# Performance work log

Hardware: AMD Instinct MI355X
Metric: run time of the kernel (lower is better)

## Reference

```python
import jax, jax.numpy as jnp
import numpy as np

N_NODES = 50000
N_EDGES = 600000
F_IN = 128
HID = 128
LN_EPS = 1e-5


def setup_inputs() -> dict:
    key = jax.random.key(0)
    ks = jax.random.split(key, 8)
    x = jax.random.normal(ks[0], (N_NODES, F_IN), dtype=jnp.float32)
    edge_index = jax.random.randint(ks[1], (2, N_EDGES), 0, N_NODES, dtype=jnp.int64)
    s1 = 1.0 / np.sqrt(F_IN)
    s2 = 1.0 / np.sqrt(HID)
    return {
        "x": x,
        "edge_index": edge_index,
        "W1": jax.random.normal(ks[2], (F_IN, HID), dtype=jnp.float32) * s1,
        "b1": jnp.zeros((HID,), dtype=jnp.float32),
        "g1": jnp.ones((HID,), dtype=jnp.float32),
        "be1": jnp.zeros((HID,), dtype=jnp.float32),
        "W2": jax.random.normal(ks[3], (HID, HID), dtype=jnp.float32) * s2,
        "b2": jnp.zeros((HID,), dtype=jnp.float32),
        "g2": jnp.ones((HID,), dtype=jnp.float32),
        "be2": jnp.zeros((HID,), dtype=jnp.float32),
    }


def _layer_norm(h, g, b):
    mu = jnp.mean(h, axis=-1, keepdims=True)
    var = jnp.mean(jnp.square(h - mu), axis=-1, keepdims=True)
    return (h - mu) * jax.lax.rsqrt(var + LN_EPS) * g + b


def reference(x, edge_index, W1, b1, g1, be1, W2, b2, g2, be2):
    n = x.shape[0]
    src, dst = edge_index[0], edge_index[1]
    # GCN symmetric normalization with self-loops: deg = in-degree(A) + 1
    deg = jax.ops.segment_sum(jnp.ones_like(src, dtype=x.dtype), dst, num_segments=n) + 1.0
    dinv = jax.lax.rsqrt(deg)                       # D^{-1/2}, [N]
    enorm = (dinv[src] * dinv[dst])[:, None]        # per-edge norm, [E,1]
    self_norm = (dinv * dinv)[:, None]              # self-loop norm,  [N,1]

    def gcn(h, W, b):
        h = h @ W                                   # [N,HID]
        agg = jax.ops.segment_sum(h[src] * enorm, dst, num_segments=n)
        return agg + h * self_norm + b

    h = jax.nn.relu(_layer_norm(gcn(x, W1, b1), g1, be1))
    h = jax.nn.relu(_layer_norm(gcn(h, W2, b2), g2, be2))
    return h  # dropout is identity in eval; LSTM evolution only runs in training
```

## Files before the change

### kernel.cpp

```cpp
#include <hip/hip_runtime.h>

#define N_NODES 50000
#define N_EDGES 600000
#define HID 128
#define LN_EPS 1e-5f
#define NB_GEMM1 782
#define NB_HIST 2344

typedef __attribute__((ext_vector_type(8))) short short8;
typedef __attribute__((ext_vector_type(4))) float f32x4;

__device__ inline float b2f(unsigned short u) {
    union { unsigned int i; float f; } v;
    v.i = ((unsigned int)u) << 16;
    return v.f;
}
__device__ inline unsigned short f2b(float f) {
    union { float f; unsigned int u; } v; v.f = f;
    unsigned int r = (v.u + 0x7FFFu + ((v.u >> 16) & 1u)) >> 16;
    return (unsigned short)r;
}

__global__ __launch_bounds__(256) void k_fused1(const float* __restrict__ x,
                                                const float* __restrict__ W1,
                                                const float* __restrict__ W2,
                                                const int* __restrict__ ei,
                                                int* __restrict__ counts,
                                                unsigned short* __restrict__ WT2,
                                                unsigned short* __restrict__ hb) {
    const int tid = threadIdx.x;

    if (blockIdx.x >= NB_GEMM1) {
        const int bi = blockIdx.x - NB_GEMM1;
        const int e = bi * 256 + tid;
        if (e < N_EDGES) atomicAdd(&counts[ei[N_EDGES + e]], 1);
        if (bi < 64) {
            const int i = bi * 256 + tid;
            const int k = i >> 7, n = i & 127;
            WT2[n * 128 + k] = f2b(W2[i]);
        }
        return;
    }

    __shared__ unsigned short wt[16384];
    {
        const float4* W4 = (const float4*)W1;
#pragma unroll
        for (int it = 0; it < 16; ++it) {
            const int i4 = tid + 256 * it;
            const float4 v = W4[i4];
            const int k  = (i4 * 4) >> 7;
            const int n0 = (i4 * 4) & 127;
            wt[(n0 + 0) * 128 + (k ^ (((n0 + 0) & 7) << 3))] = f2b(v.x);
            wt[(n0 + 1) * 128 + (k ^ (((n0 + 1) & 7) << 3))] = f2b(v.y);
            wt[(n0 + 2) * 128 + (k ^ (((n0 + 2) & 7) << 3))] = f2b(v.z);
            wt[(n0 + 3) * 128 + (k ^ (((n0 + 3) & 7) << 3))] = f2b(v.w);
        }
    }
    __syncthreads();

    const int lane = tid & 63;
    const int ln   = lane & 15;
    const int quad = lane >> 4;
    const int m0   = blockIdx.x * 64 + (tid >> 6) * 16;

    f32x4 acc[8];
#pragma unroll
    for (int t = 0; t < 8; ++t) acc[t] = (f32x4){0.f, 0.f, 0.f, 0.f};

    int arow = m0 + ln;
    if (arow >= N_NODES) arow = N_NODES - 1;
    const float* aptr = x + (size_t)arow * HID + quad * 8;

#pragma unroll
    for (int ks = 0; ks < 4; ++ks) {
        const float4 v0 = *(const float4*)(aptr + ks * 32);
        const float4 v1 = *(const float4*)(aptr + ks * 32 + 4);
        short8 a;
        a[0] = (short)f2b(v0.x); a[1] = (short)f2b(v0.y);
        a[2] = (short)f2b(v0.z); a[3] = (short)f2b(v0.w);
        a[4] = (short)f2b(v1.x); a[5] = (short)f2b(v1.y);
        a[6] = (short)f2b(v1.z); a[7] = (short)f2b(v1.w);
#pragma unroll
        for (int t = 0; t < 8; ++t) {
            const int n = t * 16 + ln;
            const short8 b = *(const short8*)&wt[n * 128 + ((quad * 8 + ks * 32) ^ ((n & 7) << 3))];
            acc[t] = __builtin_amdgcn_mfma_f32_16x16x32_bf16(a, b, acc[t], 0, 0, 0);
        }
    }

#pragma unroll
    for (int t = 0; t < 8; ++t) {
#pragma unroll
        for (int r = 0; r < 4; ++r) {
            const int row = m0 + quad * 4 + r;
            if (row < N_NODES) hb[(size_t)row * HID + t * 16 + ln] = f2b(acc[t][r]);
        }
    }
}

__global__ __launch_bounds__(256) void k_slab(const int* __restrict__ counts,
                                              int* __restrict__ gtotal,
                                              int* __restrict__ slab,
                                              float* __restrict__ dinv) {
    const int idx  = blockIdx.x * 256 + threadIdx.x;
    const int lane = threadIdx.x & 63;
    const int c = (idx < N_NODES) ? counts[idx] : 0;

    int incl = c;
#pragma unroll
    for (int off = 1; off < 64; off <<= 1) {
        int n = __shfl_up(incl, off);
        if (lane >= off) incl += n;
    }
    const int wtot = __shfl(incl, 63);
    int base = 0;
    if (lane == 0) base = atomicAdd(gtotal, wtot);
    base = __shfl(base, 0);

    if (idx < N_NODES) {
        slab[idx] = base + incl - c;
        dinv[idx] = rsqrtf((float)c + 1.0f);
    }
}

__global__ __launch_bounds__(256) void k_place(const int* __restrict__ ei,
                                               int* __restrict__ slab,
                                               int* __restrict__ esrc) {
    int e = blockIdx.x * 256 + threadIdx.x;
    if (e < N_EDGES) {
        const int d = ei[N_EDGES + e];
        const int pos = atomicAdd(&slab[d], 1);
        esrc[pos] = ei[e];
    }
}

template <bool FUSE>
__global__ __launch_bounds__(256) void k_agg(const int* __restrict__ slab_end,
                                             const int* __restrict__ counts,
                                             const int* __restrict__ esrc,
                                             const unsigned short* __restrict__ h,
                                             const float* __restrict__ dinv,
                                             const float* __restrict__ bia,
                                             const float* __restrict__ g,
                                             const float* __restrict__ be,
                                             const unsigned short* __restrict__ WT2,
                                             unsigned short* __restrict__ hb2,
                                             float* __restrict__ outf) {
    __shared__ unsigned short tile[2048];
    const int tid  = threadIdx.x;
    const int wv   = tid >> 6;
    const int lane = tid & 63;
    const int grp  = lane >> 4;
    const int fl   = lane & 15;
    const int r    = wv * 4 + grp;
    const int row  = blockIdx.x * 16 + r;

    const int e1 = slab_end[row];
    const int e0 = e1 - counts[row];

    float acc[8];
#pragma unroll
    for (int j = 0; j < 8; ++j) acc[j] = 0.f;

    int e = e0;
    for (; e + 1 < e1; e += 2) {
        const int sA = esrc[e];
        const int sB = esrc[e + 1];
        const float wA = dinv[sA];
        const float wB = dinv[sB];
        const short8 vA = *(const short8*)(h + (size_t)sA * HID + 8 * fl);
        const short8 vB = *(const short8*)(h + (size_t)sB * HID + 8 * fl);
#pragma unroll
        for (int j = 0; j < 8; ++j) {
            acc[j] = fmaf(wA, b2f((unsigned short)vA[j]), acc[j]);
            acc[j] = fmaf(wB, b2f((unsigned short)vB[j]), acc[j]);
        }
    }
    if (e < e1) {
        const int sA = esrc[e];
        const float wA = dinv[sA];
        const short8 vA = *(const short8*)(h + (size_t)sA * HID + 8 * fl);
#pragma unroll
        for (int j = 0; j < 8; ++j)
            acc[j] = fmaf(wA, b2f((unsigned short)vA[j]), acc[j]);
    }

    const float dd = dinv[row];
    const float sn = dd * dd;
    const short8 hv = *(const short8*)(h + (size_t)row * HID + 8 * fl);
    const float4 b0 = *(const float4*)(bia + 8 * fl);
    const float4 b1 = *(const float4*)(bia + 8 * fl + 4);
    const float bb[8] = {b0.x, b0.y, b0.z, b0.w, b1.x, b1.y, b1.z, b1.w};

    float v[8], s = 0.f, ss = 0.f;
#pragma unroll
    for (int j = 0; j < 8; ++j) {
        v[j] = dd * acc[j] + b2f((unsigned short)hv[j]) * sn + bb[j];
        s += v[j];
        ss = fmaf(v[j], v[j], ss);
    }

#pragma unroll
    for (int off = 1; off <= 8; off <<= 1) {
        s  += __shfl_xor(s, off);
        ss += __shfl_xor(ss, off);
    }
    const float mu  = s * (1.0f / 128.0f);
    const float var = ss * (1.0f / 128.0f) - mu * mu;
    const float rs  = rsqrtf(var + LN_EPS);

    const float4 g0  = *(const float4*)(g + 8 * fl);
    const float4 g1  = *(const float4*)(g + 8 * fl + 4);
    const float4 e0v = *(const float4*)(be + 8 * fl);
    const float4 e1v = *(const float4*)(be + 8 * fl + 4);
    const float gg[8] = {g0.x, g0.y, g0.z, g0.w, g1.x, g1.y, g1.z, g1.w};
    const float ee[8] = {e0v.x, e0v.y, e0v.z, e0v.w, e1v.x, e1v.y, e1v.z, e1v.w};
    float o[8];
#pragma unroll
    for (int j = 0; j < 8; ++j)
        o[j] = fmaxf((v[j] - mu) * rs * gg[j] + ee[j], 0.0f);

    if constexpr (!FUSE) {
        float4 w0 = {o[0], o[1], o[2], o[3]};
        float4 w1 = {o[4], o[5], o[6], o[7]};
        *(float4*)(outf + (size_t)row * HID + 8 * fl) = w0;
        *(float4*)(outf + (size_t)row * HID + 8 * fl + 4) = w1;
    } else {
        short8 w;
#pragma unroll
        for (int j = 0; j < 8; ++j) w[j] = (short)f2b(o[j]);
        *(short8*)&tile[r * 128 + ((8 * fl) ^ ((r & 7) << 3))] = w;
        __syncthreads();

        f32x4 c0 = (f32x4){0.f, 0.f, 0.f, 0.f};
        f32x4 c1 = (f32x4){0.f, 0.f, 0.f, 0.f};
        const int n0 = (wv * 2) * 16 + fl;
#pragma unroll
        for (int ks = 0; ks < 4; ++ks) {
            const short8 a = *(const short8*)&tile[fl * 128 + ((grp * 8 + ks * 32) ^ ((fl & 7) << 3))];
            const short8 bf0 = *(const short8*)(WT2 + (size_t)n0 * HID + grp * 8 + ks * 32);
            c0 = __builtin_amdgcn_mfma_f32_16x16x32_bf16(a, bf0, c0, 0, 0, 0);
            const short8 bf1 = *(const short8*)(WT2 + (size_t)(n0 + 16) * HID + grp * 8 + ks * 32);
            c1 = __builtin_amdgcn_mfma_f32_16x16x32_bf16(a, bf1, c1, 0, 0, 0);
        }
#pragma unroll
        for (int rr = 0; rr < 4; ++rr) {
            const int orow = blockIdx.x * 16 + grp * 4 + rr;
            hb2[(size_t)orow * HID + n0]      = f2b(c0[rr]);
            hb2[(size_t)orow * HID + n0 + 16] = f2b(c1[rr]);
        }
    }
}

extern "C" void kernel_launch(void* const* d_in, const int* in_sizes, int n_in,
                              void* d_out, int out_size, void* d_ws, size_t ws_size,
                              hipStream_t stream) {
    (void)in_sizes; (void)n_in; (void)out_size; (void)ws_size;

    const float* x   = (const float*)d_in[0];
    const int*   ei  = (const int*)d_in[1];
    const float* W1  = (const float*)d_in[2];
    const float* b1  = (const float*)d_in[3];
    const float* g1  = (const float*)d_in[4];
    const float* be1 = (const float*)d_in[5];
    const float* W2  = (const float*)d_in[6];
    const float* b2  = (const float*)d_in[7];
    const float* g2  = (const float*)d_in[8];
    const float* be2 = (const float*)d_in[9];
    float* out = (float*)d_out;

    int* counts = (int*)d_ws;
    int* gtotal = counts + N_NODES;
    int* slab   = (int*)d_ws + 50016;
    float* dinv = (float*)((int*)d_ws + 100016);
    int* esrc   = (int*)d_ws + 150016;
    unsigned short* WT2 = (unsigned short*)((int*)d_ws + 750016);
    unsigned short* hb  = (unsigned short*)((int*)d_ws + 758208);
    unsigned short* hb2 = (unsigned short*)((int*)d_ws + 3958208);

    hipMemsetAsync(counts, 0, (N_NODES + 1) * sizeof(int), stream);
    k_fused1<<<NB_GEMM1 + NB_HIST, 256, 0, stream>>>(x, W1, W2, ei, counts, WT2, hb);
    k_slab<<<(N_NODES + 255) / 256, 256, 0, stream>>>(counts, gtotal, slab, dinv);
    k_place<<<NB_HIST, 256, 0, stream>>>(ei, slab, esrc);

    k_agg<true><<<N_NODES / 16, 256, 0, stream>>>(slab, counts, esrc, hb, dinv,
                                                  b1, g1, be1, WT2, hb2, nullptr);
    k_agg<false><<<N_NODES / 16, 256, 0, stream>>>(slab, counts, esrc, hb2, dinv,
                                                   b2, g2, be2, nullptr, nullptr, out);
}
```

Baseline: 223.7 us.

## Merge all stages into one persistent kernel with grid-wide barriers

Replaces the five separate kernel launches (GEMM+histogram, scan, placement, two aggregation layers) with a single persistent kernel of 512 blocks that loops over work and uses atomic-counter grid barriers between phases. This removes launch overhead and inter-kernel gaps. In exchange, the GEMM and aggregation work is spread over fewer blocks with grid-stride loops, and the software barriers rely on all 512 blocks being co-resident. Spin-waiting and reduced parallelism per phase could hurt throughput.

New measurement: 566.7 us. 2.53x slower.

```diff
diff --git a/kernel.cpp b/kernel.cpp
--- a/kernel.cpp
+++ b/kernel.cpp
@@ -4,8 +4,10 @@
 #define N_EDGES 600000
 #define HID 128
 #define LN_EPS 1e-5f
-#define NB_GEMM1 782
-#define NB_HIST 2344
+#define GRID 512
+#define NTHREADS (GRID * 256)
+#define NB_GEMM 782
+#define NTILES 3125
 
 typedef __attribute__((ext_vector_type(8))) short short8;
 typedef __attribute__((ext_vector_type(4))) float f32x4;
@@ -21,140 +23,38 @@
     return (unsigned short)r;
 }
 
-__global__ __launch_bounds__(256) void k_fused1(const float* __restrict__ x,
-                                                const float* __restrict__ W1,
-                                                const float* __restrict__ W2,
-                                                const int* __restrict__ ei,
-                                                int* __restrict__ counts,
-                                                unsigned short* __restrict__ WT2,
-                                                unsigned short* __restrict__ hb) {
-    const int tid = threadIdx.x;
-
-    if (blockIdx.x >= NB_GEMM1) {
-        const int bi = blockIdx.x - NB_GEMM1;
-        const int e = bi * 256 + tid;
-        if (e < N_EDGES) atomicAdd(&counts[ei[N_EDGES + e]], 1);
-        if (bi < 64) {
-            const int i = bi * 256 + tid;
-            const int k = i >> 7, n = i & 127;
-            WT2[n * 128 + k] = f2b(W2[i]);
-        }
-        return;
-    }
-
-    __shared__ unsigned short wt[16384];
-    {
-        const float4* W4 = (const float4*)W1;
-#pragma unroll
-        for (int it = 0; it < 16; ++it) {
-            const int i4 = tid + 256 * it;
-            const float4 v = W4[i4];
-            const int k  = (i4 * 4) >> 7;
-            const int n0 = (i4 * 4) & 127;
-            wt[(n0 + 0) * 128 + (k ^ (((n0 + 0) & 7) << 3))] = f2b(v.x);
-            wt[(n0 + 1) * 128 + (k ^ (((n0 + 1) & 7) << 3))] = f2b(v.y);
-            wt[(n0 + 2) * 128 + (k ^ (((n0 + 2) & 7) << 3))] = f2b(v.z);
-            wt[(n0 + 3) * 128 + (k ^ (((n0 + 3) & 7) << 3))] = f2b(v.w);
-        }
-    }
+__device__ inline void gsync(int* bar, int target) {
     __syncthreads();
-
-    const int lane = tid & 63;
-    const int ln   = lane & 15;
-    const int quad = lane >> 4;
-    const int m0   = blockIdx.x * 64 + (tid >> 6) * 16;
-
-    f32x4 acc[8];
-#pragma unroll
-    for (int t = 0; t < 8; ++t) acc[t] = (f32x4){0.f, 0.f, 0.f, 0.f};
-
-    int arow = m0 + ln;
-    if (arow >= N_NODES) arow = N_NODES - 1;
-    const float* aptr = x + (size_t)arow * HID + quad * 8;
-
-#pragma unroll
-    for (int ks = 0; ks < 4; ++ks) {
-        const float4 v0 = *(const float4*)(aptr + ks * 32);
-        const float4 v1 = *(const float4*)(aptr + ks * 32 + 4);
-        short8 a;
-        a[0] = (short)f2b(v0.x); a[1] = (short)f2b(v0.y);
-        a[2] = (short)f2b(v0.z); a[3] = (short)f2b(v0.w);
-        a[4] = (short)f2b(v1.x); a[5] = (short)f2b(v1.y);
-        a[6] = (short)f2b(v1.z); a[7] = (short)f2b(v1.w);
-#pragma unroll
-        for (int t = 0; t < 8; ++t) {
-            const int n = t * 16 + ln;
-            const short8 b = *(const short8*)&wt[n * 128 + ((quad * 8 + ks * 32) ^ ((n & 7) << 3))];
-            acc[t] = __builtin_amdgcn_mfma_f32_16x16x32_bf16(a, b, acc[t], 0, 0, 0);
-        }
-    }
-
-#pragma unroll
-    for (int t = 0; t < 8; ++t) {
-#pragma unroll
-        for (int r = 0; r < 4; ++r) {
-            const int row = m0 + quad * 4 + r;
-            if (row < N_NODES) hb[(size_t)row * HID + t * 16 + ln] = f2b(acc[t][r]);
-        }
-    }
-}
-
-__global__ __launch_bounds__(256) void k_slab(const int* __restrict__ counts,
-                                              int* __restrict__ gtotal,
-                                              int* __restrict__ slab,
-                                              float* __restrict__ dinv) {
-    const int idx  = blockIdx.x * 256 + threadIdx.x;
-    const int lane = threadIdx.x & 63;
-    const int c = (idx < N_NODES) ? counts[idx] : 0;
-
-    int incl = c;
-#pragma unroll
-    for (int off = 1; off < 64; off <<= 1) {
-        int n = __shfl_up(incl, off);
-        if (lane >= off) incl += n;
-    }
-    const int wtot = __shfl(incl, 63);
-    int base = 0;
-    if (lane == 0) base = atomicAdd(gtotal, wtot);
-    base = __shfl(base, 0);
-
-    if (idx < N_NODES) {
-        slab[idx] = base + incl - c;
-        dinv[idx] = rsqrtf((float)c + 1.0f);
-    }
-}
-
-__global__ __launch_bounds__(256) void k_place(const int* __restrict__ ei,
-                                               int* __restrict__ slab,
-                                               int* __restrict__ esrc) {
-    int e = blockIdx.x * 256 + threadIdx.x;
-    if (e < N_EDGES) {
-        const int d = ei[N_EDGES + e];
-        const int pos = atomicAdd(&slab[d], 1);
-        esrc[pos] = ei[e];
-    }
+    if (threadIdx.x == 0) {
+        __threadfence();
+        atomicAdd(bar, 1);
+        while (atomicAdd(bar, 0) < target)
+            __builtin_amdgcn_s_sleep(8);
+        __threadfence();
+    }
+    __syncthreads();
 }
 
 template <bool FUSE>
-__global__ __launch_bounds__(256) void k_agg(const int* __restrict__ slab_end,
-                                             const int* __restrict__ counts,
-                                             const int* __restrict__ esrc,
-                                             const unsigned short* __restrict__ h,
-                                             const float* __restrict__ dinv,
-                                             const float* __restrict__ bia,
-                                             const float* __restrict__ g,
-                                             const float* __restrict__ be,
-                                             const unsigned short* __restrict__ WT2,
-                                             unsigned short* __restrict__ hb2,
-                                             float* __restrict__ outf) {
-    __shared__ unsigned short tile[2048];
-    const int tid  = threadIdx.x;
+__device__ __forceinline__ void agg_tile(const int tileid, const int tid,
+                                         const int* __restrict__ slab_end,
+                                         const int* __restrict__ counts,
+                                         const int* __restrict__ esrc,
+                                         const unsigned short* __restrict__ h,
+                                         const float* __restrict__ dinv,
+                                         const float* __restrict__ bia,
+                                         const float* __restrict__ g,
+                                         const float* __restrict__ be,
+                                         const unsigned short* __restrict__ WT2,
+                                         unsigned short* __restrict__ hb2,
+                                         float* __restrict__ outf,
+                                         unsigned short* smem) {
     const int wv   = tid >> 6;
     const int lane = tid & 63;
     const int grp  = lane >> 4;
     const int fl   = lane & 15;
     const int r    = wv * 4 + grp;
-    const int row  = blockIdx.x * 16 + r;
+    const int row  = tileid * 16 + r;
 
     const int e1 = slab_end[row];
     const int e0 = e1 - counts[row];
@@ -230,7 +130,7 @@
         short8 w;
 #pragma unroll
         for (int j = 0; j < 8; ++j) w[j] = (short)f2b(o[j]);
-        *(short8*)&tile[r * 128 + ((8 * fl) ^ ((r & 7) << 3))] = w;
+        *(short8*)&smem[r * 128 + ((8 * fl) ^ ((r & 7) << 3))] = w;
         __syncthreads();
 
         f32x4 c0 = (f32x4){0.f, 0.f, 0.f, 0.f};
@@ -238,7 +138,7 @@
         const int n0 = (wv * 2) * 16 + fl;
 #pragma unroll
         for (int ks = 0; ks < 4; ++ks) {
-            const short8 a = *(const short8*)&tile[fl * 128 + ((grp * 8 + ks * 32) ^ ((fl & 7) << 3))];
+            const short8 a = *(const short8*)&smem[fl * 128 + ((grp * 8 + ks * 32) ^ ((fl & 7) << 3))];
             const short8 bf0 = *(const short8*)(WT2 + (size_t)n0 * HID + grp * 8 + ks * 32);
             c0 = __builtin_amdgcn_mfma_f32_16x16x32_bf16(a, bf0, c0, 0, 0, 0);
             const short8 bf1 = *(const short8*)(WT2 + (size_t)(n0 + 16) * HID + grp * 8 + ks * 32);
@@ -246,11 +146,136 @@
         }
 #pragma unroll
         for (int rr = 0; rr < 4; ++rr) {
-            const int orow = blockIdx.x * 16 + grp * 4 + rr;
+            const int orow = tileid * 16 + grp * 4 + rr;
             hb2[(size_t)orow * HID + n0]      = f2b(c0[rr]);
             hb2[(size_t)orow * HID + n0 + 16] = f2b(c1[rr]);
         }
-    }
+        __syncthreads();
+    }
+}
+
+__global__ __launch_bounds__(256, 4) void k_mega(
+        const float* __restrict__ x, const int* __restrict__ ei,
+        const float* __restrict__ W1, const float* __restrict__ b1,
+        const float* __restrict__ g1, const float* __restrict__ be1,
+        const float* __restrict__ W2, const float* __restrict__ b2,
+        const float* __restrict__ g2, const float* __restrict__ be2,
+        int* __restrict__ counts, int* __restrict__ gtotal, int* bar,
+        int* __restrict__ slab, float* __restrict__ dinv,
+        int* __restrict__ esrc, unsigned short* __restrict__ WT2,
+        unsigned short* __restrict__ hb, unsigned short* __restrict__ hb2,
+        float* __restrict__ out) {
+    __shared__ unsigned short smem[16384];
+    const int tid  = threadIdx.x;
+    const int gtid = blockIdx.x * 256 + tid;
+
+    if (gtid < 16384) {
+        const int k = gtid >> 7, n = gtid & 127;
+        WT2[n * 128 + k] = f2b(W2[gtid]);
+    }
+
+    {
+        const float4* W4 = (const float4*)W1;
+#pragma unroll
+        for (int it = 0; it < 16; ++it) {
+            const int i4 = tid + 256 * it;
+            const float4 v = W4[i4];
+            const int k  = (i4 * 4) >> 7;
+            const int n0 = (i4 * 4) & 127;
+            smem[(n0 + 0) * 128 + (k ^ (((n0 + 0) & 7) << 3))] = f2b(v.x);
+            smem[(n0 + 1) * 128 + (k ^ (((n0 + 1) & 7) << 3))] = f2b(v.y);
+            smem[(n0 + 2) * 128 + (k ^ (((n0 + 2) & 7) << 3))] = f2b(v.z);
+            smem[(n0 + 3) * 128 + (k ^ (((n0 + 3) & 7) << 3))] = f2b(v.w);
+        }
+    }
+    __syncthreads();
+
+    {
+        const int lane = tid & 63;
+        const int ln   = lane & 15;
+        const int quad = lane >> 4;
+        for (int mt = blockIdx.x; mt < NB_GEMM; mt += GRID) {
+            const int m0 = mt * 64 + (tid >> 6) * 16;
+
+            f32x4 acc[8];
+#pragma unroll
+            for (int t = 0; t < 8; ++t) acc[t] = (f32x4){0.f, 0.f, 0.f, 0.f};
+
+            int arow = m0 + ln;
+            if (arow >= N_NODES) arow = N_NODES - 1;
+            const float* aptr = x + (size_t)arow * HID + quad * 8;
+
+#pragma unroll
+            for (int ks = 0; ks < 4; ++ks) {
+                const float4 v0 = *(const float4*)(aptr + ks * 32);
+                const float4 v1 = *(const float4*)(aptr + ks * 32 + 4);
+                short8 a;
+                a[0] = (short)f2b(v0.x); a[1] = (short)f2b(v0.y);
+                a[2] = (short)f2b(v0.z); a[3] = (short)f2b(v0.w);
+                a[4] = (short)f2b(v1.x); a[5] = (short)f2b(v1.y);
+                a[6] = (short)f2b(v1.z); a[7] = (short)f2b(v1.w);
+#pragma unroll
+                for (int t = 0; t < 8; ++t) {
+                    const int n = t * 16 + ln;
+                    const short8 b = *(const short8*)&smem[n * 128 + ((quad * 8 + ks * 32) ^ ((n & 7) << 3))];
+                    acc[t] = __builtin_amdgcn_mfma_f32_16x16x32_bf16(a, b, acc[t], 0, 0, 0);
+                }
+            }
+
+#pragma unroll
+            for (int t = 0; t < 8; ++t) {
+#pragma unroll
+                for (int rr = 0; rr < 4; ++rr) {
+                    const int row = m0 + quad * 4 + rr;
+                    if (row < N_NODES) hb[(size_t)row * HID + t * 16 + ln] = f2b(acc[t][rr]);
+                }
+            }
+        }
+    }
+
+    for (int e = gtid; e < N_EDGES; e += NTHREADS)
+        atomicAdd(&counts[ei[N_EDGES + e]], 1);
+
+    gsync(bar, GRID);
+
+    {
+        const int lane = tid & 63;
+        if (gtid - lane < N_NODES) {
+            const int c = (gtid < N_NODES) ? counts[gtid] : 0;
+            int incl = c;
+#pragma unroll
+            for (int off = 1; off < 64; off <<= 1) {
+                int nn = __shfl_up(incl, off);
+                if (lane >= off) incl += nn;
+            }
+            const int wtot = __shfl(incl, 63);
+            int base = 0;
+            if (lane == 0) base = atomicAdd(gtotal, wtot);
+            base = __shfl(base, 0);
+            if (gtid < N_NODES) {
+                slab[gtid] = base + incl - c;
+                dinv[gtid] = rsqrtf((float)c + 1.0f);
+            }
+        }
+    }
+
+    gsync(bar, 2 * GRID);
+
+    for (int e = gtid; e < N_EDGES; e += NTHREADS) {
+        const int d = ei[N_EDGES + e];
+        const int pos = atomicAdd(&slab[d], 1);
+        esrc[pos] = ei[e];
+    }
+
+    gsync(bar, 3 * GRID);
+
+    for (int t = blockIdx.x; t < NTILES; t += GRID)
+        agg_tile<true>(t, tid, slab, counts, esrc, hb, dinv, b1, g1, be1, WT2, hb2, nullptr, smem);
+
+    gsync(bar, 4 * GRID);
+
+    for (int t = blockIdx.x; t < NTILES; t += GRID)
+        agg_tile<false>(t, tid, slab, counts, esrc, hb2, dinv, b2, g2, be2, nullptr, nullptr, out, smem);
 }
 
 extern "C" void kernel_launch(void* const* d_in, const int* in_sizes, int n_in,
@@ -272,6 +297,7 @@
 
     int* counts = (int*)d_ws;
     int* gtotal = counts + N_NODES;
+    int* bar    = counts + N_NODES + 1;
     int* slab   = (int*)d_ws + 50016;
     float* dinv = (float*)((int*)d_ws + 100016);
     int* esrc   = (int*)d_ws + 150016;
@@ -279,13 +305,8 @@
     unsigned short* hb  = (unsigned short*)((int*)d_ws + 758208);
     unsigned short* hb2 = (unsigned short*)((int*)d_ws + 3958208);
 
-    hipMemsetAsync(counts, 0, (N_NODES + 1) * sizeof(int), stream);
-    k_fused1<<<NB_GEMM1 + NB_HIST, 256, 0, stream>>>(x, W1, W2, ei, counts, WT2, hb);
-    k_slab<<<(N_NODES + 255) / 256, 256, 0, stream>>>(counts, gtotal, slab, dinv);
-    k_place<<<NB_HIST, 256, 0, stream>>>(ei, slab, esrc);
-
-    k_agg<true><<<N_NODES / 16, 256, 0, stream>>>(slab, counts, esrc, hb, dinv,
-                                                  b1, g1, be1, WT2, hb2, nullptr);
-    k_agg<false><<<N_NODES / 16, 256, 0, stream>>>(slab, counts, esrc, hb2, dinv,
-                                                   b2, g2, be2, nullptr, nullptr, out);
-}
+    hipMemsetAsync(counts, 0, (N_NODES + 2) * sizeof(int), stream);
+    k_mega<<<GRID, 256, 0, stream>>>(x, ei, W1, b1, g1, be1, W2, b2, g2, be2,
+                                     counts, gtotal, bar, slab, dinv, esrc,
+                                     WT2, hb, hb2, out);
+}
```
